# Optimization experiments

Measured on AMD Instinct MI355X. Metric: run time of the kernel, lower is better.

The kernel has to match this reference:

```python
import jax, jax.numpy as jnp
import numpy as np

B, J, D = 64, 512, 1024

def setup_inputs() -> dict:
    key = jax.random.key(0)
    k_x, k_m, k1, k2, k3 = jax.random.split(key, 5)
    x = jax.random.normal(k_x, (B, J, D), dtype=jnp.float32)
    mask = (jax.random.uniform(k_m, (B, J)) > 0.1).astype(jnp.float32)
    s1 = 1.0 / np.sqrt(D)
    W1 = jax.random.uniform(k1, (D, D), minval=-s1, maxval=s1, dtype=jnp.float32)
    b1 = jnp.zeros((D,), jnp.float32)
    W2 = jax.random.uniform(k2, (D, 1), minval=-s1, maxval=s1, dtype=jnp.float32)
    b2 = jnp.zeros((1,), jnp.float32)
    W3 = jax.random.uniform(k3, (D, 3), minval=-s1, maxval=s1, dtype=jnp.float32)
    b3 = jnp.zeros((3,), jnp.float32)
    return {"x": x, "mask": mask, "W1": W1, "b1": b1, "W2": W2, "b2": b2, "W3": W3, "b3": b3}

def reference(x, mask, W1, b1, W2, b2, W3, b3):
    # MLP attention scoring: linear1 -> tanh -> linear2 -> sigmoid
    h = jnp.tanh(jnp.einsum('bjd,de->bje', x, W1) + b1)          # [B,J,D]
    val = jax.nn.sigmoid(jnp.einsum('bjd,do->bjo', h, W2) + b2)  # [B,J,1]
    val = val * mask[:, :, None]                                  # mask out pads
    inv_sum = 1.0 / jnp.sum(val, axis=(1, 2))                     # [B]
    att_weights = val * inv_sum[:, None, None]                    # [B,J,1]
    pooled = jnp.einsum('bjk,bjm->bk', x, att_weights)            # [B,D]
    output_val = pooled @ W3 + b3                                 # [B,3]
    return output_val, att_weights
```

## Files before the change

kernel.cpp:

```cpp
#include <hip/hip_runtime.h>
#include <math.h>
#include <stdint.h>

#define B_ 64
#define J_ 512
#define D_ 1024

typedef __attribute__((ext_vector_type(8))) short short8;
typedef __attribute__((ext_vector_type(4))) float f32x4;

#define GLOBAL_AS __attribute__((address_space(1)))
#define LDS_AS    __attribute__((address_space(3)))

__device__ __forceinline__ void async16(const void* g, void* l) {
    __builtin_amdgcn_global_load_lds((const GLOBAL_AS uint32_t*)g,
                                     (LDS_AS uint32_t*)l, 16, 0, 0);
}

__device__ __forceinline__ float fast_tanh(float x) {
    return 1.0f - 2.0f / (1.0f + __expf(2.0f * x));
}

__device__ __forceinline__ unsigned short f2bf(float f) {
    uint32_t u = __builtin_bit_cast(uint32_t, f);
    u += 0x7fffu + ((u >> 16) & 1u);
    return (unsigned short)(u >> 16);
}

__global__ __launch_bounds__(256) void cast_x_kernel(const float* __restrict__ x,
                                                     unsigned short* __restrict__ xb) {
    const size_t i = ((size_t)blockIdx.x * 256 + threadIdx.x) * 8;
    const float4 v0 = *reinterpret_cast<const float4*>(x + i);
    const float4 v1 = *reinterpret_cast<const float4*>(x + i + 4);
    uint4 o;
    o.x = (uint32_t)f2bf(v0.x) | ((uint32_t)f2bf(v0.y) << 16);
    o.y = (uint32_t)f2bf(v0.z) | ((uint32_t)f2bf(v0.w) << 16);
    o.z = (uint32_t)f2bf(v1.x) | ((uint32_t)f2bf(v1.y) << 16);
    o.w = (uint32_t)f2bf(v1.z) | ((uint32_t)f2bf(v1.w) << 16);
    *reinterpret_cast<uint4*>(xb + i) = o;
}

__global__ __launch_bounds__(256) void prep_kernel(const float* __restrict__ W1,
                                                   unsigned short* __restrict__ W1t,
                                                   float* __restrict__ pooled) {
    __shared__ float t[32][33];
    const int b   = blockIdx.x;
    const int tid = threadIdx.x;
    if (b < 256) pooled[b * 256 + tid] = 0.f;
    const int bx = b & 31, by = b >> 5;
    const int tx = tid & 31, ty = tid >> 5;
    const int n = bx * 32 + tx;
    for (int i = ty; i < 32; i += 8)
        t[i][tx] = W1[(size_t)(by * 32 + i) * D_ + n];
    __syncthreads();
    const int k = by * 32 + tx;
    for (int i = ty; i < 32; i += 8)
        W1t[(size_t)(bx * 32 + i) * D_ + k] = f2bf(t[tx][i]);
}

__global__ __launch_bounds__(512, 4) void gemm_score_kernel(
    const unsigned short* __restrict__ Xb, const unsigned short* __restrict__ W1t,
    const float* __restrict__ b1, const float* __restrict__ W2,
    const float* __restrict__ b2, const float* __restrict__ mask,
    float* __restrict__ val_ws, float* __restrict__ pooled)
{
    __shared__ __align__(16) unsigned short ldsA[64 * 64];
    __shared__ __align__(16) unsigned short ldsB[512 * 64];

    const int tid  = threadIdx.x;
    const int wave = tid >> 6;
    const int l    = tid & 63;
    const int l15  = l & 15;
    const int kgrp = l >> 4;
    const int l7   = l & 7;
    const int r0   = blockIdx.x * 64;
    const int bb   = r0 >> 9;

    const int arow = tid >> 3;
    const unsigned short* gA = Xb + (size_t)(r0 + arow) * D_
                                  + (((tid & 7) ^ (arow & 7)) << 3);
    unsigned short* lA = ldsA + (wave << 9);

    const unsigned short* gB0 = W1t + (size_t)arow * D_
                                    + (((tid & 7) ^ (arow & 7)) << 3);
    unsigned short* lB0 = ldsB + (wave << 9);

    int abase[2], bbase[2];
    #pragma unroll
    for (int ks = 0; ks < 2; ++ks) {
        const int swz = (((ks * 4 + kgrp) ^ l7) << 3);
        abase[ks] = l15 * 64 + swz;
        bbase[ks] = (wave * 64 + l15) * 64 + swz;
    }

    float pv[4][4];
    #pragma unroll
    for (int mi = 0; mi < 4; ++mi)
        #pragma unroll
        for (int r = 0; r < 4; ++r) pv[mi][r] = 0.f;

    for (int n0 = 0; n0 < 2; ++n0) {
        f32x4 acc[4][4];
        #pragma unroll
        for (int mi = 0; mi < 4; ++mi)
            #pragma unroll
            for (int ni = 0; ni < 4; ++ni)
                acc[mi][ni] = (f32x4){0.f, 0.f, 0.f, 0.f};

        const size_t bofs = (size_t)n0 * 512 * D_;
        for (int k0 = 0; k0 < D_; k0 += 64) {
            async16(gA + k0, lA);
            #pragma unroll
            for (int t = 0; t < 8; ++t)
                async16(gB0 + bofs + (size_t)t * 64 * D_ + k0, lB0 + t * 4096);
            __syncthreads();
            #pragma unroll
            for (int ks = 0; ks < 2; ++ks) {
                const short8 a0 = *reinterpret_cast<const short8*>(ldsA + abase[ks]);
                const short8 a1 = *reinterpret_cast<const short8*>(ldsA + abase[ks] + 1024);
                const short8 a2 = *reinterpret_cast<const short8*>(ldsA + abase[ks] + 2048);
                const short8 a3 = *reinterpret_cast<const short8*>(ldsA + abase[ks] + 3072);
                #pragma unroll
                for (int ni = 0; ni < 4; ++ni) {
                    const short8 bv = *reinterpret_cast<const short8*>(
                        ldsB + bbase[ks] + ni * 1024);
                    acc[0][ni] = __builtin_amdgcn_mfma_f32_16x16x32_bf16(a0, bv, acc[0][ni], 0, 0, 0);
                    acc[1][ni] = __builtin_amdgcn_mfma_f32_16x16x32_bf16(a1, bv, acc[1][ni], 0, 0, 0);
                    acc[2][ni] = __builtin_amdgcn_mfma_f32_16x16x32_bf16(a2, bv, acc[2][ni], 0, 0, 0);
                    acc[3][ni] = __builtin_amdgcn_mfma_f32_16x16x32_bf16(a3, bv, acc[3][ni], 0, 0, 0);
                }
            }
            __syncthreads();
        }

        #pragma unroll
        for (int ni = 0; ni < 4; ++ni) {
            const int col = n0 * 512 + wave * 64 + ni * 16 + l15;
            const float b1v = b1[col];
            const float w2v = W2[col];
            #pragma unroll
            for (int mi = 0; mi < 4; ++mi)
                #pragma unroll
                for (int r = 0; r < 4; ++r) {
                    const float h = fast_tanh(acc[mi][ni][r] + b1v);
                    pv[mi][r] = fmaf(h, w2v, pv[mi][r]);
                }
        }
    }

    float* pv_part = reinterpret_cast<float*>(ldsB);
    float* vrow    = pv_part + 512;

    #pragma unroll
    for (int mi = 0; mi < 4; ++mi)
        #pragma unroll
        for (int r = 0; r < 4; ++r) {
            float s = pv[mi][r];
            s += __shfl_xor(s, 1);
            s += __shfl_xor(s, 2);
            s += __shfl_xor(s, 4);
            s += __shfl_xor(s, 8);
            if (l15 == 0) pv_part[wave * 64 + mi * 16 + kgrp * 4 + r] = s;
        }
    __syncthreads();
    if (tid < 64) {
        float s = b2[0];
        #pragma unroll
        for (int w = 0; w < 8; ++w) s += pv_part[w * 64 + tid];
        const float sg = 1.0f / (1.0f + __expf(-s));
        const float v = sg * mask[r0 + tid];
        val_ws[r0 + tid] = v;
        vrow[tid] = v;
    }
    __syncthreads();

    const int kc = tid << 1;
    float a0 = 0.f, a1 = 0.f;
    for (int row = 0; row < 64; ++row) {
        const float v = vrow[row];
        const uint32_t u = *reinterpret_cast<const uint32_t*>(
            Xb + (size_t)(r0 + row) * D_ + kc);
        a0 = fmaf(__builtin_bit_cast(float, u << 16), v, a0);
        a1 = fmaf(__builtin_bit_cast(float, u & 0xffff0000u), v, a1);
    }
    atomicAdd(&pooled[bb * D_ + kc], a0);
    atomicAdd(&pooled[bb * D_ + kc + 1], a1);
}

#define MT 64
#define KT 32
#define PAD 68

__global__ __launch_bounds__(256) void score_kernel_fp32(
    const float* __restrict__ x, const float* __restrict__ mask,
    const float* __restrict__ W1, const float* __restrict__ b1,
    const float* __restrict__ W2, const float* __restrict__ b2,
    float* __restrict__ val_ws, float* __restrict__ pooled)
{
    __shared__ float As[KT][PAD];
    __shared__ float Bs[KT][PAD];
    __shared__ float red[MT][17];
    __shared__ float vrow[MT];

    const int tid = threadIdx.x;
    const int tx = tid & 15;
    const int ty = tid >> 4;
    const int r0 = blockIdx.x * MT;
    const int b  = r0 >> 9;

    float pv[4] = {0.f, 0.f, 0.f, 0.f};

    for (int n0 = 0; n0 < D_; n0 += 64) {
        float acc[4][4];
        #pragma unroll
        for (int i = 0; i < 4; ++i)
            #pragma unroll
            for (int j = 0; j < 4; ++j) acc[i][j] = 0.f;

        for (int k0 = 0; k0 < D_; k0 += KT) {
            #pragma unroll
            for (int ll = 0; ll < 2; ++ll) {
                const int f   = tid + ll * 256;
                const int row = f >> 3;
                const int k4  = (f & 7) << 2;
                const float4 xv = *reinterpret_cast<const float4*>(
                    &x[(size_t)(r0 + row) * D_ + k0 + k4]);
                As[k4 + 0][row] = xv.x;
                As[k4 + 1][row] = xv.y;
                As[k4 + 2][row] = xv.z;
                As[k4 + 3][row] = xv.w;
            }
            #pragma unroll
            for (int ll = 0; ll < 2; ++ll) {
                const int f  = tid + ll * 256;
                const int k  = f >> 4;
                const int n4 = (f & 15) << 2;
                const float4 wv = *reinterpret_cast<const float4*>(
                    &W1[(size_t)(k0 + k) * D_ + n0 + n4]);
                *reinterpret_cast<float4*>(&Bs[k][n4]) = wv;
            }
            __syncthreads();
            #pragma unroll
            for (int kk = 0; kk < KT; ++kk) {
                const float4 a4 = *reinterpret_cast<const float4*>(&As[kk][ty << 2]);
                const float4 b4 = *reinterpret_cast<const float4*>(&Bs[kk][tx << 2]);
                const float av[4] = {a4.x, a4.y, a4.z, a4.w};
                const float bv[4] = {b4.x, b4.y, b4.z, b4.w};
                #pragma unroll
                for (int i = 0; i < 4; ++i)
                    #pragma unroll
                    for (int j = 0; j < 4; ++j)
                        acc[i][j] = fmaf(av[i], bv[j], acc[i][j]);
            }
            __syncthreads();
        }
        #pragma unroll
        for (int j = 0; j < 4; ++j) {
            const int col = n0 + (tx << 2) + j;
            const float b1v = b1[col];
            const float w2v = W2[col];
            #pragma unroll
            for (int i = 0; i < 4; ++i) {
                const float h = fast_tanh(acc[i][j] + b1v);
                pv[i] = fmaf(h, w2v, pv[i]);
            }
        }
    }

    #pragma unroll
    for (int i = 0; i < 4; ++i) red[(ty << 2) + i][tx] = pv[i];
    __syncthreads();

    if (tid < MT) {
        float s = 0.f;
        #pragma unroll
        for (int t = 0; t < 16; ++t) s += red[tid][t];
        const float z  = s + b2[0];
        const float sg = 1.0f / (1.0f + __expf(-z));
        const float v  = sg * mask[r0 + tid];
        val_ws[r0 + tid] = v;
        vrow[tid] = v;
    }
    __syncthreads();

    const int k = tid << 2;
    float a0 = 0.f, a1 = 0.f, a2 = 0.f, a3 = 0.f;
    for (int row = 0; row < MT; ++row) {
        const float v = vrow[row];
        const float4 xv = *reinterpret_cast<const float4*>(
            &x[(size_t)(r0 + row) * D_ + k]);
        a0 = fmaf(xv.x, v, a0);
        a1 = fmaf(xv.y, v, a1);
        a2 = fmaf(xv.z, v, a2);
        a3 = fmaf(xv.w, v, a3);
    }
    float* pb = &pooled[b * D_ + k];
    atomicAdd(pb + 0, a0);
    atomicAdd(pb + 1, a1);
    atomicAdd(pb + 2, a2);
    atomicAdd(pb + 3, a3);
}

__global__ __launch_bounds__(256) void finalize_kernel(
    const float* __restrict__ val_ws, const float* __restrict__ pooled,
    const float* __restrict__ W3, const float* __restrict__ b3,
    float* __restrict__ out)
{
    __shared__ float sred[256];
    const int b = blockIdx.x;
    const int tid = threadIdx.x;

    const float v0 = val_ws[b * J_ + tid];
    const float v1 = val_ws[b * J_ + 256 + tid];
    sred[tid] = v0 + v1;
    __syncthreads();
    for (int s = 128; s > 0; s >>= 1) {
        if (tid < s) sred[tid] += sred[tid + s];
        __syncthreads();
    }
    const float inv = 1.0f / sred[0];

    out[192 + b * J_ + tid]       = v0 * inv;
    out[192 + b * J_ + 256 + tid] = v1 * inv;

    const int k = tid << 2;
    float acc3[3] = {0.f, 0.f, 0.f};
    #pragma unroll
    for (int c = 0; c < 4; ++c) {
        const float p = pooled[b * D_ + k + c] * inv;
        acc3[0] = fmaf(p, W3[(k + c) * 3 + 0], acc3[0]);
        acc3[1] = fmaf(p, W3[(k + c) * 3 + 1], acc3[1]);
        acc3[2] = fmaf(p, W3[(k + c) * 3 + 2], acc3[2]);
    }
    for (int o = 0; o < 3; ++o) {
        __syncthreads();
        sred[tid] = acc3[o];
        __syncthreads();
        for (int s = 128; s > 0; s >>= 1) {
            if (tid < s) sred[tid] += sred[tid + s];
            __syncthreads();
        }
        if (tid == 0) out[b * 3 + o] = sred[0] + b3[o];
    }
}

extern "C" void kernel_launch(void* const* d_in, const int* in_sizes, int n_in,
                              void* d_out, int out_size, void* d_ws, size_t ws_size,
                              hipStream_t stream) {
    const float* x    = (const float*)d_in[0];
    const float* mask = (const float*)d_in[1];
    const float* W1   = (const float*)d_in[2];
    const float* b1   = (const float*)d_in[3];
    const float* W2   = (const float*)d_in[4];
    const float* b2   = (const float*)d_in[5];
    const float* W3   = (const float*)d_in[6];
    const float* b3   = (const float*)d_in[7];
    float* out = (float*)d_out;

    const size_t XB_BYTES   = (size_t)B_ * J_ * D_ * 2;
    const size_t W1T_BYTES  = (size_t)D_ * D_ * 2;
    const size_t VAL_BYTES  = (size_t)B_ * J_ * 4;
    const size_t POOL_BYTES = (size_t)B_ * D_ * 4;
    const size_t NEED = XB_BYTES + W1T_BYTES + VAL_BYTES + POOL_BYTES;

    if (ws_size >= NEED) {
        unsigned short* Xb  = (unsigned short*)d_ws;
        unsigned short* W1t = (unsigned short*)((char*)d_ws + XB_BYTES);
        float* val_ws = (float*)((char*)d_ws + XB_BYTES + W1T_BYTES);
        float* pooled = (float*)((char*)d_ws + XB_BYTES + W1T_BYTES + VAL_BYTES);

        prep_kernel<<<1024, 256, 0, stream>>>(W1, W1t, pooled);
        cast_x_kernel<<<(B_ * J_ * D_) / (256 * 8), 256, 0, stream>>>(x, Xb);
        gemm_score_kernel<<<512, 512, 0, stream>>>(Xb, W1t, b1, W2, b2, mask,
                                                   val_ws, pooled);
        finalize_kernel<<<B_, 256, 0, stream>>>(val_ws, pooled, W3, b3, out);
    } else {
        float* val_ws = (float*)d_ws;
        float* pooled = val_ws + B_ * J_;
        hipMemsetAsync(pooled, 0, POOL_BYTES, stream);
        score_kernel_fp32<<<(B_ * J_) / MT, 256, 0, stream>>>(
            x, mask, W1, b1, W2, b2, val_ws, pooled);
        finalize_kernel<<<B_, 256, 0, stream>>>(val_ws, pooled, W3, b3, out);
    }
}
```

Measured before the change: 300.3 us.

## Fuse fp32-to-bf16 cast of x into GEMM A-tile load with register prefetch

```diff
diff --git a/kernel.cpp b/kernel.cpp
--- a/kernel.cpp
+++ b/kernel.cpp
@@ -27,17 +27,8 @@
     return (unsigned short)(u >> 16);
 }
 
-__global__ __launch_bounds__(256) void cast_x_kernel(const float* __restrict__ x,
-                                                     unsigned short* __restrict__ xb) {
-    const size_t i = ((size_t)blockIdx.x * 256 + threadIdx.x) * 8;
-    const float4 v0 = *reinterpret_cast<const float4*>(x + i);
-    const float4 v1 = *reinterpret_cast<const float4*>(x + i + 4);
-    uint4 o;
-    o.x = (uint32_t)f2bf(v0.x) | ((uint32_t)f2bf(v0.y) << 16);
-    o.y = (uint32_t)f2bf(v0.z) | ((uint32_t)f2bf(v0.w) << 16);
-    o.z = (uint32_t)f2bf(v1.x) | ((uint32_t)f2bf(v1.y) << 16);
-    o.w = (uint32_t)f2bf(v1.z) | ((uint32_t)f2bf(v1.w) << 16);
-    *reinterpret_cast<uint4*>(xb + i) = o;
+__device__ __forceinline__ uint32_t pk2(float a, float b) {
+    return (uint32_t)f2bf(a) | ((uint32_t)f2bf(b) << 16);
 }
 
 __global__ __launch_bounds__(256) void prep_kernel(const float* __restrict__ W1,
@@ -59,7 +50,7 @@
 }
 
 __global__ __launch_bounds__(512, 4) void gemm_score_kernel(
-    const unsigned short* __restrict__ Xb, const unsigned short* __restrict__ W1t,
+    const float* __restrict__ x, const unsigned short* __restrict__ W1t,
     const float* __restrict__ b1, const float* __restrict__ W2,
     const float* __restrict__ b2, const float* __restrict__ mask,
     float* __restrict__ val_ws, float* __restrict__ pooled)
@@ -77,12 +68,10 @@
     const int bb   = r0 >> 9;
 
     const int arow = tid >> 3;
-    const unsigned short* gA = Xb + (size_t)(r0 + arow) * D_
-                                  + (((tid & 7) ^ (arow & 7)) << 3);
-    unsigned short* lA = ldsA + (wave << 9);
-
-    const unsigned short* gB0 = W1t + (size_t)arow * D_
-                                    + (((tid & 7) ^ (arow & 7)) << 3);
+    const int ach  = ((tid & 7) ^ (arow & 7)) << 3;
+    const float* gAx = x + (size_t)(r0 + arow) * D_ + ach;
+
+    const unsigned short* gB0 = W1t + (size_t)arow * D_ + ach;
     unsigned short* lB0 = ldsB + (wave << 9);
 
     int abase[2], bbase[2];
@@ -99,6 +88,15 @@
         #pragma unroll
         for (int r = 0; r < 4; ++r) pv[mi][r] = 0.f;
 
+    uint4 curA;
+    {
+        const float4 p0 = *reinterpret_cast<const float4*>(gAx);
+        const float4 p1 = *reinterpret_cast<const float4*>(gAx + 4);
+        curA = (uint4){pk2(p0.x, p0.y), pk2(p0.z, p0.w),
+                       pk2(p1.x, p1.y), pk2(p1.z, p1.w)};
+    }
+
+    #pragma unroll
     for (int n0 = 0; n0 < 2; ++n0) {
         f32x4 acc[4][4];
         #pragma unroll
@@ -109,11 +107,16 @@
 
         const size_t bofs = (size_t)n0 * 512 * D_;
         for (int k0 = 0; k0 < D_; k0 += 64) {
-            async16(gA + k0, lA);
+            *reinterpret_cast<uint4*>(ldsA + tid * 8) = curA;
             #pragma unroll
             for (int t = 0; t < 8; ++t)
                 async16(gB0 + bofs + (size_t)t * 64 * D_ + k0, lB0 + t * 4096);
             __syncthreads();
+
+            const int nk = (k0 == D_ - 64) ? 0 : k0 + 64;
+            const float4 q0 = *reinterpret_cast<const float4*>(gAx + nk);
+            const float4 q1 = *reinterpret_cast<const float4*>(gAx + nk + 4);
+
             #pragma unroll
             for (int ks = 0; ks < 2; ++ks) {
                 const short8 a0 = *reinterpret_cast<const short8*>(ldsA + abase[ks]);
@@ -130,6 +133,9 @@
                     acc[3][ni] = __builtin_amdgcn_mfma_f32_16x16x32_bf16(a3, bv, acc[3][ni], 0, 0, 0);
                 }
             }
+
+            curA = (uint4){pk2(q0.x, q0.y), pk2(q0.z, q0.w),
+                           pk2(q1.x, q1.y), pk2(q1.z, q1.w)};
             __syncthreads();
         }
 
@@ -178,10 +184,10 @@
     float a0 = 0.f, a1 = 0.f;
     for (int row = 0; row < 64; ++row) {
         const float v = vrow[row];
-        const uint32_t u = *reinterpret_cast<const uint32_t*>(
-            Xb + (size_t)(r0 + row) * D_ + kc);
-        a0 = fmaf(__builtin_bit_cast(float, u << 16), v, a0);
-        a1 = fmaf(__builtin_bit_cast(float, u & 0xffff0000u), v, a1);
+        const float2 xv = *reinterpret_cast<const float2*>(
+            x + (size_t)(r0 + row) * D_ + kc);
+        a0 = fmaf(xv.x, v, a0);
+        a1 = fmaf(xv.y, v, a1);
     }
     atomicAdd(&pooled[bb * D_ + kc], a0);
     atomicAdd(&pooled[bb * D_ + kc + 1], a1);
@@ -357,21 +363,18 @@
     const float* b3   = (const float*)d_in[7];
     float* out = (float*)d_out;
 
-    const size_t XB_BYTES   = (size_t)B_ * J_ * D_ * 2;
     const size_t W1T_BYTES  = (size_t)D_ * D_ * 2;
     const size_t VAL_BYTES  = (size_t)B_ * J_ * 4;
     const size_t POOL_BYTES = (size_t)B_ * D_ * 4;
-    const size_t NEED = XB_BYTES + W1T_BYTES + VAL_BYTES + POOL_BYTES;
+    const size_t NEED = W1T_BYTES + VAL_BYTES + POOL_BYTES;
 
     if (ws_size >= NEED) {
-        unsigned short* Xb  = (unsigned short*)d_ws;
-        unsigned short* W1t = (unsigned short*)((char*)d_ws + XB_BYTES);
-        float* val_ws = (float*)((char*)d_ws + XB_BYTES + W1T_BYTES);
-        float* pooled = (float*)((char*)d_ws + XB_BYTES + W1T_BYTES + VAL_BYTES);
+        unsigned short* W1t = (unsigned short*)d_ws;
+        float* val_ws = (float*)((char*)d_ws + W1T_BYTES);
+        float* pooled = (float*)((char*)d_ws + W1T_BYTES + VAL_BYTES);
 
         prep_kernel<<<1024, 256, 0, stream>>>(W1, W1t, pooled);
-        cast_x_kernel<<<(B_ * J_ * D_) / (256 * 8), 256, 0, stream>>>(x, Xb);
-        gemm_score_kernel<<<512, 512, 0, stream>>>(Xb, W1t, b1, W2, b2, mask,
+        gemm_score_kernel<<<512, 512, 0, stream>>>(x, W1t, b1, W2, b2, mask,
                                                    val_ws, pooled);
         finalize_kernel<<<B_, 256, 0, stream>>>(val_ws, pooled, W3, b3, out);
     } else {
```

Result: slower. 308.1 us (+2.6%).
